# Optimization experiments

Measured on AMD Instinct MI355X. Metric: run time of the kernel, lower is better.

Reference implementation:

```python
import jax, jax.numpy as jnp
import numpy as np

N_NODES = 100000
N_EDGES = 1600000
N_GRAPHS = 512
IN_F, H1, H2 = 128, 128, 256
N_GROUPS, N_FAM = 16, 10


def setup_inputs() -> dict:
    key = jax.random.key(0)
    ks = jax.random.split(key, 8)
    x = jax.random.normal(ks[0], (N_NODES, IN_F), dtype=jnp.float32)
    edge_index = jax.random.randint(ks[1], (2, N_EDGES), 0, N_NODES, dtype=jnp.int64)
    batch = jnp.sort(jax.random.randint(ks[2], (N_NODES,), 0, N_GRAPHS, dtype=jnp.int64))
    W1 = jax.random.normal(ks[3], (IN_F, H1), dtype=jnp.float32) / np.sqrt(IN_F)
    b1 = jnp.zeros((H1,), dtype=jnp.float32)
    W2 = jax.random.normal(ks[4], (H1, H2), dtype=jnp.float32) / np.sqrt(H1)
    b2 = jnp.zeros((H2,), dtype=jnp.float32)
    Wg = jax.random.normal(ks[5], (H2, N_GROUPS), dtype=jnp.float32) / np.sqrt(H2)
    bg = jnp.zeros((N_GROUPS,), dtype=jnp.float32)
    Wf = jax.random.normal(ks[6], (N_GROUPS, H2, N_FAM), dtype=jnp.float32) / np.sqrt(H2)
    bf = jnp.zeros((N_GROUPS, N_FAM), dtype=jnp.float32)
    return {"x": x, "edge_index": edge_index, "batch": batch,
            "W1": W1, "b1": b1, "W2": W2, "b2": b2,
            "Wg": Wg, "bg": bg, "Wf": Wf, "bf": bf}


def gcn_conv(x, W, b, src, dst, num_nodes):
    # PyG GCNConv: add self-loops, symmetric normalization, scatter-add aggregation.
    xw = x @ W  # [N, out]
    deg = jax.ops.segment_sum(jnp.ones((src.shape[0],), x.dtype), dst,
                              num_segments=num_nodes) + 1.0  # +1 self-loop
    dinv = jax.lax.rsqrt(deg)
    coef = dinv[src] * dinv[dst]            # [E]
    msg = xw[src] * coef[:, None]           # gather + scale (memory-bound)
    agg = jax.ops.segment_sum(msg, dst, num_segments=num_nodes)
    agg = agg + xw * (dinv * dinv)[:, None]  # self-loop contribution
    return agg + b


def reference(x, edge_index, batch, W1, b1, W2, b2, Wg, bg, Wf, bf):
    src, dst = edge_index[0], edge_index[1]
    h = jax.nn.relu(gcn_conv(x, W1, b1, src, dst, N_NODES))
    # dropout p=0.5 is identity in eval mode
    h = gcn_conv(h, W2, b2, src, dst, N_NODES)
    # global mean pool over graphs
    sums = jax.ops.segment_sum(h, batch, num_segments=N_GRAPHS)       # [G, H2]
    cnts = jax.ops.segment_sum(jnp.ones((N_NODES,), h.dtype), batch,
                               num_segments=N_GRAPHS)
    pooled = sums / jnp.maximum(cnts, 1.0)[:, None]
    group_logits = pooled @ Wg + bg                                   # [G, num_groups]
    family_logits = jnp.einsum('bd,gdf->gbf', pooled, Wf) + bf[:, None, :]
    return group_logits, family_logits
```

## Files before the change

kernel.cpp:

```cpp
#include <hip/hip_runtime.h>

#define NN 100000
#define NE 1600000
#define NGR 512
#define KF 128
#define H2F 256
#define NGRP 16
#define NFAM 10

#define CH 128
#define NCHUNK ((NN + CH - 1) / CH)
#define PT 6656
#define NT ((NE + PT - 1) / PT)
#define PREPB_BLKS 64

#define NSPLIT 8

typedef __attribute__((ext_vector_type(8))) short short8;
typedef __attribute__((ext_vector_type(4))) float floatx4;
typedef __attribute__((ext_vector_type(2))) float floatx2;

__device__ __forceinline__ unsigned short f2bf(float f) {
  unsigned u = __float_as_uint(f);
  unsigned r = (u + 0x7fff + ((u >> 16) & 1)) >> 16;
  return (unsigned short)r;
}
__device__ __forceinline__ unsigned short pk_fp8(float a, float b) {
  return (unsigned short)__builtin_amdgcn_cvt_pk_fp8_f32(a, b, 0, false);
}
__device__ __forceinline__ floatx2 unpk_fp8(unsigned short u) {
  return __builtin_amdgcn_cvt_pk_f32_fp8((int)u, false);
}


__global__ __launch_bounds__(256) void k_histprep(const int* __restrict__ ei,
                                                  int* __restrict__ tot,
                                                  const float* __restrict__ W,
                                                  unsigned short* __restrict__ Bp) {
  __shared__ int lh[NCHUNK];
  int tid = threadIdx.x;
  if (blockIdx.x >= NT) {
    int idx = (blockIdx.x - NT) * 256 + tid;
    int j = idx & 7;
    int l = (idx >> 3) & 63;
    int rest = idx >> 9;
    int nc = rest & 7;
    int kc = rest >> 3;
    int k = kc * 32 + (l >> 4) * 8 + j;
    int nn = nc * 16 + (l & 15);
    Bp[idx] = f2bf(W[k * KF + nn]);
    return;
  }
  for (int g = tid; g < NCHUNK; g += 256) lh[g] = 0;
  __syncthreads();
  int base = blockIdx.x * PT;
  int nv = min(PT, NE - base);
  for (int i = tid; i < nv; i += 256) atomicAdd(&lh[ei[NE + base + i] >> 7], 1);
  __syncthreads();
  for (int g = tid; g < NCHUNK; g += 256) {
    int v = lh[g];
    if (v) atomicAdd(&tot[g], v);
  }
}


__global__ __launch_bounds__(256) void k_scantot(const int* __restrict__ tot,
                                                 int* __restrict__ cbase,
                                                 int* __restrict__ cursor) {
  __shared__ int ssc[256];
  int tid = threadIdx.x;
  int v4[4]; int loc = 0;
#pragma unroll
  for (int j = 0; j < 4; ++j) {
    int idx = tid * 4 + j;
    v4[j] = (idx < NCHUNK) ? tot[idx] : 0;
    loc += v4[j];
  }
  ssc[tid] = loc;
  __syncthreads();
  for (int off = 1; off < 256; off <<= 1) {
    int val = (tid >= off) ? ssc[tid - off] : 0;
    __syncthreads();
    ssc[tid] += val;
    __syncthreads();
  }
  int excl = ssc[tid] - loc;
#pragma unroll
  for (int j = 0; j < 4; ++j) {
    int idx = tid * 4 + j;
    if (idx < NCHUNK) { cbase[idx] = excl; cursor[idx] = excl; }
    excl += v4[j];
  }
  if (tid == 255) cbase[NCHUNK] = excl;
}


__global__ __launch_bounds__(256) void k_pscatter(const int* __restrict__ ei,
                                                  int* __restrict__ cursor,
                                                  int2* __restrict__ erec) {
  __shared__ int2 stage[PT];
  __shared__ int lstart[NCHUNK];
  __shared__ int lrun[NCHUNK];
  __shared__ int gbase[NCHUNK];
  __shared__ int ssc[256];
  int t0 = blockIdx.x, tid = threadIdx.x;
  for (int g = tid; g < NCHUNK; g += 256) lrun[g] = 0;
  __syncthreads();
  int base = t0 * PT;
  int nv = min(PT, NE - base);
  for (int i = tid; i < nv; i += 256) atomicAdd(&lrun[ei[NE + base + i] >> 7], 1);
  __syncthreads();
  int v4[4]; int loc = 0;
#pragma unroll
  for (int j = 0; j < 4; ++j) {
    int idx = tid * 4 + j;
    v4[j] = (idx < NCHUNK) ? lrun[idx] : 0;
    loc += v4[j];
  }
  ssc[tid] = loc;
  __syncthreads();
  for (int off = 1; off < 256; off <<= 1) {
    int val = (tid >= off) ? ssc[tid - off] : 0;
    __syncthreads();
    ssc[tid] += val;
    __syncthreads();
  }
  int excl = ssc[tid] - loc;
#pragma unroll
  for (int j = 0; j < 4; ++j) {
    int idx = tid * 4 + j;
    if (idx < NCHUNK) lstart[idx] = excl;
    excl += v4[j];
  }
  __syncthreads();
  for (int g = tid; g < NCHUNK; g += 256) {
    int cnt = ((g + 1 < NCHUNK) ? lstart[g + 1] : nv) - lstart[g];
    gbase[g] = cnt ? atomicAdd(&cursor[g], cnt) : 0;
    lrun[g] = lstart[g];
  }
  __syncthreads();
  for (int i = tid; i < nv; i += 256) {
    int s = ei[base + i], d = ei[NE + base + i];
    int pos = atomicAdd(&lrun[d >> 7], 1);
    stage[pos] = make_int2(s, d);
  }
  __syncthreads();
  for (int j = tid; j < nv; j += 256) {
    int2 r = stage[j];
    int g = r.y >> 7;
    erec[gbase[g] + (j - lstart[g])] = r;
  }
}


__global__ __launch_bounds__(256) void k_sort(const int2* __restrict__ erec,
                                              const int* __restrict__ cbase,
                                              int* __restrict__ esrc,
                                              float* __restrict__ ew,
                                              int* __restrict__ rowptr,
                                              float* __restrict__ dinv) {
  __shared__ int hist[CH];
  __shared__ int lrun[CH];
  __shared__ float ldv[CH];
  __shared__ int sc[256];
  const int c = blockIdx.x, tid = threadIdx.x;
  const int e0 = cbase[c], e1 = cbase[c + 1];
  const int nv = e1 - e0;
  if (tid < CH) hist[tid] = 0;
  __syncthreads();
  for (int i = tid; i < nv; i += 256) atomicAdd(&hist[erec[e0 + i].y & (CH - 1)], 1);
  __syncthreads();
  int deg = (tid < CH) ? hist[tid] : 0;
  sc[tid] = deg;
  __syncthreads();
  for (int off = 1; off < 256; off <<= 1) {
    int val = (tid >= off) ? sc[tid - off] : 0;
    __syncthreads();
    sc[tid] += val;
    __syncthreads();
  }
  int excl = sc[tid] - deg;
  int node = c * CH + tid;
  if (tid < CH) {
    lrun[tid] = excl;
    if (node < NN) {
      float dv = rsqrtf((float)(deg + 1));
      rowptr[node] = e0 + excl;
      dinv[node] = dv;
      ldv[tid] = dv;
    } else if (node == NN) {
      rowptr[NN] = e0 + excl;
    }
  }
  __syncthreads();
  for (int i = tid; i < nv; i += 256) {
    int2 r = erec[e0 + i];
    int ln = r.y & (CH - 1);
    int pos = atomicAdd(&lrun[ln], 1);
    esrc[e0 + pos] = r.x;
    ew[e0 + pos] = ldv[ln];
  }
}


__global__ __launch_bounds__(256) void k_gemm_mfma(const float* __restrict__ A,
                                                   const unsigned short* __restrict__ Bp,
                                                   const float* __restrict__ dinv,
                                                   unsigned short* __restrict__ C) {
  constexpr int K = 128;
  constexpr int NCH = KF / 16;
  const int wv = blockIdx.x * 4 + (threadIdx.x >> 6);
  const int row0 = wv * 16;
  if (row0 >= NN) return;
  const int lane = threadIdx.x & 63;
  const int m = lane & 15;
  const int q = lane >> 4;

  floatx4 acc[NCH];
#pragma unroll
  for (int i = 0; i < NCH; ++i) acc[i] = (floatx4){0.f, 0.f, 0.f, 0.f};

  const int arow = row0 + m;
#pragma unroll
  for (int kc = 0; kc < 4; ++kc) {
    const float* ap = A + (size_t)arow * K + kc * 32 + q * 8;
    float4 f0 = *(const float4*)ap;
    float4 f1 = *(const float4*)(ap + 4);
    short8 af;
    af[0] = (short)f2bf(f0.x); af[1] = (short)f2bf(f0.y);
    af[2] = (short)f2bf(f0.z); af[3] = (short)f2bf(f0.w);
    af[4] = (short)f2bf(f1.x); af[5] = (short)f2bf(f1.y);
    af[6] = (short)f2bf(f1.z); af[7] = (short)f2bf(f1.w);
    const unsigned short* bp = Bp + (size_t)kc * NCH * 512;
#pragma unroll
    for (int nc = 0; nc < NCH; ++nc) {
      short8 bfr = *(const short8*)(bp + (size_t)nc * 512 + lane * 8);
      acc[nc] = __builtin_amdgcn_mfma_f32_16x16x32_bf16(af, bfr, acc[nc], 0, 0, 0);
    }
  }

  float ds[4];
#pragma unroll
  for (int r = 0; r < 4; ++r) ds[r] = dinv[row0 + q * 4 + r];
#pragma unroll
  for (int nc = 0; nc < 4; ++nc) {
#pragma unroll
    for (int r = 0; r < 4; ++r) {
      int row = row0 + q * 4 + r;
      C[(size_t)row * 64 + nc * 16 + m] =
          pk_fp8(acc[nc][r] * ds[r], acc[nc + 4][r] * ds[r]);
    }
  }
}


__global__ __launch_bounds__(128) void k_agg1(const unsigned short* __restrict__ p,
                                              const float* __restrict__ bias,
                                              const int* __restrict__ rowptr,
                                              const int* __restrict__ esrc,
                                              const float* __restrict__ dinv,
                                              unsigned short* __restrict__ outp) {
  const int n = blockIdx.x * 2 + (threadIdx.x >> 6);
  const int t = threadIdx.x & 63;
  const int u = t & 31;
  const int half = t >> 5;
  const unsigned* __restrict__ prow = (const unsigned*)p;

  float a0 = 0.f, a1 = 0.f, a2 = 0.f, a3 = 0.f;

  if (half == 0) {
    unsigned v = prow[((unsigned)n << 5) + u];
    floatx2 lo = unpk_fp8((unsigned short)(v & 0xffffu));
    floatx2 hi = unpk_fp8((unsigned short)(v >> 16));
    a0 = lo.x; a1 = lo.y; a2 = hi.x; a3 = hi.y;
  }

  const int r0 = rowptr[n];
  const int r1 = rowptr[n + 1];
  int i = r0;

#define PAIR_TIER(NP)                                                  \
  for (; i + 2 * (NP) <= r1; i += 2 * (NP)) {                          \
    const int ib = i + half;                                           \
    unsigned s[NP];                                                    \
    _Pragma("unroll") for (int j = 0; j < (NP); ++j)                   \
        s[j] = (unsigned)esrc[ib + 2 * j];                             \
    unsigned v[NP];                                                    \
    _Pragma("unroll") for (int j = 0; j < (NP); ++j)                   \
        v[j] = prow[(s[j] << 5) + u];                                  \
    _Pragma("unroll") for (int j = 0; j < (NP); ++j) {                 \
      floatx2 lo = unpk_fp8((unsigned short)(v[j] & 0xffffu));         \
      floatx2 hi = unpk_fp8((unsigned short)(v[j] >> 16));             \
      a0 += lo.x; a1 += lo.y; a2 += hi.x; a3 += hi.y;                  \
    }                                                                  \
  }

  PAIR_TIER(8)
  PAIR_TIER(4)
  PAIR_TIER(2)
  PAIR_TIER(1)
#undef PAIR_TIER

  if (i < r1 && half == 0) {
    unsigned s = (unsigned)esrc[i];
    unsigned v = prow[(s << 5) + u];
    floatx2 lo = unpk_fp8((unsigned short)(v & 0xffffu));
    floatx2 hi = unpk_fp8((unsigned short)(v >> 16));
    a0 += lo.x; a1 += lo.y; a2 += hi.x; a3 += hi.y;
  }

  a0 += __shfl_down(a0, 32, 64);
  a1 += __shfl_down(a1, 32, 64);
  a2 += __shfl_down(a2, 32, 64);
  a3 += __shfl_down(a3, 32, 64);

  if (half == 0) {
    const float dn = dinv[n];
    float2 blo = *(const float2*)(bias + 2 * u);
    float2 bhi = *(const float2*)(bias + 64 + 2 * u);
    float x0 = fmaxf(fmaf(dn, a0, blo.x), 0.f) * dn;
    float x1 = fmaxf(fmaf(dn, a1, bhi.x), 0.f) * dn;
    float x2 = fmaxf(fmaf(dn, a2, blo.y), 0.f) * dn;
    float x3 = fmaxf(fmaf(dn, a3, bhi.y), 0.f) * dn;
    unsigned lo = pk_fp8(x0, x1);
    unsigned hi = pk_fp8(x2, x3);
    ((unsigned*)outp)[((unsigned)n << 5) + u] = lo | (hi << 16);
  }
}


__global__ __launch_bounds__(256) void k_aggpart(const unsigned short* __restrict__ p,
                                                 const int* __restrict__ batch,
                                                 const int* __restrict__ rowptr,
                                                 const int* __restrict__ esrc,
                                                 const float* __restrict__ ew,
                                                 const float* __restrict__ dinv,
                                                 float* __restrict__ pooled) {
  __shared__ float sacc[4][128];
  __shared__ int bnd[2];
  const int g = blockIdx.x / NSPLIT;
  const int part = blockIdx.x % NSPLIT;
  const int tid = threadIdx.x;
  if (tid < 2) {
    int target = g + tid;
    int lo = 0, hi = NN;
    while (lo < hi) { int mid = (lo + hi) >> 1; if (batch[mid] < target) lo = mid + 1; else hi = mid; }
    bnd[tid] = lo;
  }
  __syncthreads();
  const int start = bnd[0], end = bnd[1];
  const int wv = tid >> 6, t = tid & 63, u = t & 31, half = t >> 5;
  const unsigned* __restrict__ prow = (const unsigned*)p;

  float a0 = 0.f, a1 = 0.f, a2 = 0.f, a3 = 0.f;

  const int e0 = rowptr[start];
  const int e1 = rowptr[end];
  const int elen = e1 - e0;
  const int eper = (elen + NSPLIT - 1) / NSPLIT;
  const int is = min(e0 + part * eper, e1);
  const int ie = min(is + eper, e1);

  int i = is + wv * 2 + half;
  for (; i + 56 < ie; i += 64) {
    unsigned s[8];
    float w[8];
    unsigned v[8];
#pragma unroll
    for (int j = 0; j < 8; ++j) s[j] = (unsigned)esrc[i + 8 * j];
#pragma unroll
    for (int j = 0; j < 8; ++j) w[j] = ew[i + 8 * j];
#pragma unroll
    for (int j = 0; j < 8; ++j) v[j] = prow[(s[j] << 5) + u];
#pragma unroll
    for (int j = 0; j < 8; ++j) {
      floatx2 lo = unpk_fp8((unsigned short)(v[j] & 0xffffu));
      floatx2 hi = unpk_fp8((unsigned short)(v[j] >> 16));
      a0 = fmaf(w[j], lo.x, a0); a1 = fmaf(w[j], lo.y, a1);
      a2 = fmaf(w[j], hi.x, a2); a3 = fmaf(w[j], hi.y, a3);
    }
  }
  for (; i < ie; i += 8) {
    unsigned s_ = (unsigned)esrc[i];
    float w_ = ew[i];
    unsigned v_ = prow[(s_ << 5) + u];
    floatx2 lo = unpk_fp8((unsigned short)(v_ & 0xffffu));
    floatx2 hi = unpk_fp8((unsigned short)(v_ >> 16));
    a0 = fmaf(w_, lo.x, a0); a1 = fmaf(w_, lo.y, a1);
    a2 = fmaf(w_, hi.x, a2); a3 = fmaf(w_, hi.y, a3);
  }

  const int nlen = end - start;
  const int nper = (nlen + NSPLIT - 1) / NSPLIT;
  const int ns = min(start + part * nper, end);
  const int ne = min(ns + nper, end);
  for (int n = ns + wv * 2 + half; n < ne; n += 8) {
    float w_ = dinv[n];
    unsigned v_ = prow[((unsigned)n << 5) + u];
    floatx2 lo = unpk_fp8((unsigned short)(v_ & 0xffffu));
    floatx2 hi = unpk_fp8((unsigned short)(v_ >> 16));
    a0 = fmaf(w_, lo.x, a0); a1 = fmaf(w_, lo.y, a1);
    a2 = fmaf(w_, hi.x, a2); a3 = fmaf(w_, hi.y, a3);
  }

  a0 += __shfl_down(a0, 32, 64);
  a1 += __shfl_down(a1, 32, 64);
  a2 += __shfl_down(a2, 32, 64);
  a3 += __shfl_down(a3, 32, 64);
  if (half == 0) {
    sacc[wv][2 * u] = a0;
    sacc[wv][2 * u + 1] = a2;
    sacc[wv][2 * u + 64] = a1;
    sacc[wv][2 * u + 65] = a3;
  }
  __syncthreads();
  if (tid < KF) {
    float v = sacc[0][tid] + sacc[1][tid] + sacc[2][tid] + sacc[3][tid];
    atomicAdd(&pooled[(size_t)g * KF + tid], v);
  }
}


__global__ __launch_bounds__(256) void k_heads(const float* __restrict__ pooled,
                                               const int* __restrict__ batch,
                                               const float* __restrict__ W2,
                                               const float* __restrict__ b2,
                                               const float* __restrict__ Wg,
                                               const float* __restrict__ bg,
                                               const float* __restrict__ Wf,
                                               const float* __restrict__ bfb,
                                               float* __restrict__ out) {
  __shared__ float pr[KF];
  __shared__ float pp[H2F];
  __shared__ int bnd[2];
  const int g = blockIdx.x;
  const int tid = threadIdx.x;
  if (tid < 2) {
    int target = g + tid;
    int lo = 0, hi = NN;
    while (lo < hi) { int mid = (lo + hi) >> 1; if (batch[mid] < target) lo = mid + 1; else hi = mid; }
    bnd[tid] = lo;
  }
  __syncthreads();
  if (tid < KF) {
    float c = fmaxf((float)(bnd[1] - bnd[0]), 1.f);
    pr[tid] = pooled[(size_t)g * KF + tid] / c;
  }
  __syncthreads();
  float acc = b2[tid];
#pragma unroll 8
  for (int d = 0; d < KF; ++d) acc = fmaf(pr[d], W2[d * H2F + tid], acc);
  pp[tid] = acc;
  __syncthreads();
  if (tid < NGRP) {
    float a = bg[tid];
    for (int d = 0; d < H2F; ++d) a = fmaf(pp[d], Wg[d * NGRP + tid], a);
    out[g * NGRP + tid] = a;
  } else if (tid >= 64 && tid < 64 + NGRP * NFAM) {
    int uu = tid - 64;
    int gg = uu / NFAM;
    int ff = uu % NFAM;
    float a = bfb[gg * NFAM + ff];
    for (int d = 0; d < H2F; ++d) a = fmaf(pp[d], Wf[(gg * H2F + d) * NFAM + ff], a);
    out[NGR * NGRP + (size_t)gg * NGR * NFAM + g * NFAM + ff] = a;
  }
}


extern "C" void kernel_launch(void* const* d_in, const int* in_sizes, int n_in,
                              void* d_out, int out_size, void* d_ws, size_t ws_size,
                              hipStream_t stream) {
  const float* x    = (const float*)d_in[0];
  const int*   ei   = (const int*)d_in[1];
  const int*   batch= (const int*)d_in[2];
  const float* W1   = (const float*)d_in[3];
  const float* b1   = (const float*)d_in[4];
  const float* W2   = (const float*)d_in[5];
  const float* b2   = (const float*)d_in[6];
  const float* Wg   = (const float*)d_in[7];
  const float* bg   = (const float*)d_in[8];
  const float* Wf   = (const float*)d_in[9];
  const float* bfb  = (const float*)d_in[10];
  float* out = (float*)d_out;

  char* w = (char*)d_ws;
  auto take = [&](size_t bytes) {
    char* p = w;
    w += (bytes + 255) & ~(size_t)255;
    return (void*)p;
  };
  int*   tot   = (int*)take((size_t)NCHUNK * 4);
  float* pooled= (float*)take((size_t)NGR * KF * 4);
  int*   cbase = (int*)take((size_t)(NCHUNK + 1) * 4);
  int*   cursor= (int*)take((size_t)NCHUNK * 4);
  int2*  erec  = (int2*)take((size_t)NE * 8);
  int*   esrc  = (int*)take((size_t)NE * 4);
  float* ew    = (float*)take((size_t)NE * 4);
  int*   rowptr= (int*)take((size_t)(NN + 1) * 4);
  float* dinv  = (float*)take((size_t)NN * 4);
  unsigned short* Bp1 = (unsigned short*)take((size_t)KF * KF * 2);
  unsigned short* xw1 = (unsigned short*)take((size_t)NN * 64 * 2);
  unsigned short* h1  = (unsigned short*)take((size_t)NN * 64 * 2);

  size_t zbytes = (size_t)((char*)pooled - (char*)tot) + (size_t)NGR * KF * 4;
  hipMemsetAsync(tot, 0, zbytes, stream);

  k_histprep<<<NT + PREPB_BLKS, 256, 0, stream>>>(ei, tot, W1, Bp1);
  k_scantot<<<1, 256, 0, stream>>>(tot, cbase, cursor);
  k_pscatter<<<NT, 256, 0, stream>>>(ei, cursor, erec);
  k_sort<<<NCHUNK, 256, 0, stream>>>(erec, cbase, esrc, ew, rowptr, dinv);

  k_gemm_mfma<<<1563, 256, 0, stream>>>(x, Bp1, dinv, xw1);

  k_agg1<<<NN / 2, 128, 0, stream>>>(xw1, b1, rowptr, esrc, dinv, h1);
  k_aggpart<<<NGR * NSPLIT, 256, 0, stream>>>(h1, batch, rowptr, esrc, ew, dinv, pooled);
  k_heads<<<NGR, 256, 0, stream>>>(pooled, batch, W2, b2, Wg, bg, Wf, bfb, out);
}
```

Baseline: 292.4 us.

## Drop per-edge weight array, factor dinv per destination, precompute graph boundaries

Removes the per-edge weight array written by the sort kernel. The second aggregation now walks destination nodes via rowptr, sums the unscaled neighbour rows and multiplies once by dinv[dst], which saves one 4-byte read and write per edge. Graph boundary offsets are computed once by extra blocks in the histogram kernel instead of a binary search in every aggregation and heads block. The trade-off is that node-parallel work splitting within each graph replaces even edge-range splitting, which can leave load imbalance across high-degree nodes and uses half-wave pairing with tiered unrolling.

```diff
diff --git a/kernel.cpp b/kernel.cpp
--- a/kernel.cpp
+++ b/kernel.cpp
@@ -13,6 +13,7 @@
 #define PT 6656
 #define NT ((NE + PT - 1) / PT)
 #define PREPB_BLKS 64
+#define GBB ((NN + 255) / 256)
 
 #define NSPLIT 8
 
@@ -34,11 +35,24 @@
 
 
 __global__ __launch_bounds__(256) void k_histprep(const int* __restrict__ ei,
+                                                  const int* __restrict__ batch,
                                                   int* __restrict__ tot,
+                                                  int* __restrict__ gb,
                                                   const float* __restrict__ W,
                                                   unsigned short* __restrict__ Bp) {
   __shared__ int lh[NCHUNK];
   int tid = threadIdx.x;
+  if (blockIdx.x >= NT + PREPB_BLKS) {
+    int n = (blockIdx.x - NT - PREPB_BLKS) * 256 + tid;
+    if (n >= NN) return;
+    int b0 = batch[n];
+    if (n == 0) {
+      for (int g = 0; g <= b0; ++g) gb[g] = 0;
+    }
+    int b1 = (n + 1 < NN) ? batch[n + 1] : NGR;
+    for (int g = b0 + 1; g <= b1; ++g) gb[g] = n + 1;
+    return;
+  }
   if (blockIdx.x >= NT) {
     int idx = (blockIdx.x - NT) * 256 + tid;
     int j = idx & 7;
@@ -156,12 +170,10 @@
 __global__ __launch_bounds__(256) void k_sort(const int2* __restrict__ erec,
                                               const int* __restrict__ cbase,
                                               int* __restrict__ esrc,
-                                              float* __restrict__ ew,
                                               int* __restrict__ rowptr,
                                               float* __restrict__ dinv) {
   __shared__ int hist[CH];
   __shared__ int lrun[CH];
-  __shared__ float ldv[CH];
   __shared__ int sc[256];
   const int c = blockIdx.x, tid = threadIdx.x;
   const int e0 = cbase[c], e1 = cbase[c + 1];
@@ -184,10 +196,8 @@
   if (tid < CH) {
     lrun[tid] = excl;
     if (node < NN) {
-      float dv = rsqrtf((float)(deg + 1));
       rowptr[node] = e0 + excl;
-      dinv[node] = dv;
-      ldv[tid] = dv;
+      dinv[node] = rsqrtf((float)(deg + 1));
     } else if (node == NN) {
       rowptr[NN] = e0 + excl;
     }
@@ -195,10 +205,8 @@
   __syncthreads();
   for (int i = tid; i < nv; i += 256) {
     int2 r = erec[e0 + i];
-    int ln = r.y & (CH - 1);
-    int pos = atomicAdd(&lrun[ln], 1);
+    int pos = atomicAdd(&lrun[r.y & (CH - 1)], 1);
     esrc[e0 + pos] = r.x;
-    ew[e0 + pos] = ldv[ln];
   }
 }
 
@@ -330,77 +338,73 @@
 
 
 __global__ __launch_bounds__(256) void k_aggpart(const unsigned short* __restrict__ p,
-                                                 const int* __restrict__ batch,
+                                                 const int* __restrict__ gb,
                                                  const int* __restrict__ rowptr,
                                                  const int* __restrict__ esrc,
-                                                 const float* __restrict__ ew,
                                                  const float* __restrict__ dinv,
                                                  float* __restrict__ pooled) {
   __shared__ float sacc[4][128];
-  __shared__ int bnd[2];
   const int g = blockIdx.x / NSPLIT;
   const int part = blockIdx.x % NSPLIT;
   const int tid = threadIdx.x;
-  if (tid < 2) {
-    int target = g + tid;
-    int lo = 0, hi = NN;
-    while (lo < hi) { int mid = (lo + hi) >> 1; if (batch[mid] < target) lo = mid + 1; else hi = mid; }
-    bnd[tid] = lo;
-  }
-  __syncthreads();
-  const int start = bnd[0], end = bnd[1];
+  const int start = gb[g], end = gb[g + 1];
   const int wv = tid >> 6, t = tid & 63, u = t & 31, half = t >> 5;
   const unsigned* __restrict__ prow = (const unsigned*)p;
 
   float a0 = 0.f, a1 = 0.f, a2 = 0.f, a3 = 0.f;
-
-  const int e0 = rowptr[start];
-  const int e1 = rowptr[end];
-  const int elen = e1 - e0;
-  const int eper = (elen + NSPLIT - 1) / NSPLIT;
-  const int is = min(e0 + part * eper, e1);
-  const int ie = min(is + eper, e1);
-
-  int i = is + wv * 2 + half;
-  for (; i + 56 < ie; i += 64) {
-    unsigned s[8];
-    float w[8];
-    unsigned v[8];
-#pragma unroll
-    for (int j = 0; j < 8; ++j) s[j] = (unsigned)esrc[i + 8 * j];
-#pragma unroll
-    for (int j = 0; j < 8; ++j) w[j] = ew[i + 8 * j];
-#pragma unroll
-    for (int j = 0; j < 8; ++j) v[j] = prow[(s[j] << 5) + u];
-#pragma unroll
-    for (int j = 0; j < 8; ++j) {
-      floatx2 lo = unpk_fp8((unsigned short)(v[j] & 0xffffu));
-      floatx2 hi = unpk_fp8((unsigned short)(v[j] >> 16));
-      a0 = fmaf(w[j], lo.x, a0); a1 = fmaf(w[j], lo.y, a1);
-      a2 = fmaf(w[j], hi.x, a2); a3 = fmaf(w[j], hi.y, a3);
-    }
-  }
-  for (; i < ie; i += 8) {
-    unsigned s_ = (unsigned)esrc[i];
-    float w_ = ew[i];
-    unsigned v_ = prow[(s_ << 5) + u];
-    floatx2 lo = unpk_fp8((unsigned short)(v_ & 0xffffu));
-    floatx2 hi = unpk_fp8((unsigned short)(v_ >> 16));
-    a0 = fmaf(w_, lo.x, a0); a1 = fmaf(w_, lo.y, a1);
-    a2 = fmaf(w_, hi.x, a2); a3 = fmaf(w_, hi.y, a3);
-  }
 
   const int nlen = end - start;
   const int nper = (nlen + NSPLIT - 1) / NSPLIT;
   const int ns = min(start + part * nper, end);
   const int ne = min(ns + nper, end);
-  for (int n = ns + wv * 2 + half; n < ne; n += 8) {
-    float w_ = dinv[n];
-    unsigned v_ = prow[((unsigned)n << 5) + u];
-    floatx2 lo = unpk_fp8((unsigned short)(v_ & 0xffffu));
-    floatx2 hi = unpk_fp8((unsigned short)(v_ >> 16));
-    a0 = fmaf(w_, lo.x, a0); a1 = fmaf(w_, lo.y, a1);
-    a2 = fmaf(w_, hi.x, a2); a3 = fmaf(w_, hi.y, a3);
+
+  for (int n = ns + wv; n < ne; n += 4) {
+    float t0, t1, t2, t3;
+    if (half == 0) {
+      unsigned v = prow[((unsigned)n << 5) + u];
+      floatx2 lo = unpk_fp8((unsigned short)(v & 0xffffu));
+      floatx2 hi = unpk_fp8((unsigned short)(v >> 16));
+      t0 = lo.x; t1 = lo.y; t2 = hi.x; t3 = hi.y;
+    } else {
+      t0 = 0.f; t1 = 0.f; t2 = 0.f; t3 = 0.f;
+    }
+    const int r0 = rowptr[n];
+    const int r1 = rowptr[n + 1];
+    int i = r0;
+
+#define PAIR_TIER(NP)                                                  \
+    for (; i + 2 * (NP) <= r1; i += 2 * (NP)) {                        \
+      const int ib = i + half;                                         \
+      unsigned s[NP];                                                  \
+      _Pragma("unroll") for (int j = 0; j < (NP); ++j)                 \
+          s[j] = (unsigned)esrc[ib + 2 * j];                           \
+      unsigned v[NP];                                                  \
+      _Pragma("unroll") for (int j = 0; j < (NP); ++j)                 \
+          v[j] = prow[(s[j] << 5) + u];                                \
+      _Pragma("unroll") for (int j = 0; j < (NP); ++j) {               \
+        floatx2 lo = unpk_fp8((unsigned short)(v[j] & 0xffffu));       \
+        floatx2 hi = unpk_fp8((unsigned short)(v[j] >> 16));           \
+        t0 += lo.x; t1 += lo.y; t2 += hi.x; t3 += hi.y;                \
+      }                                                                \
+    }
+
+    PAIR_TIER(8)
+    PAIR_TIER(4)
+    PAIR_TIER(2)
+    PAIR_TIER(1)
+#undef PAIR_TIER
+
+    if (i < r1 && half == 0) {
+      unsigned s = (unsigned)esrc[i];
+      unsigned v = prow[(s << 5) + u];
+      floatx2 lo = unpk_fp8((unsigned short)(v & 0xffffu));
+      floatx2 hi = unpk_fp8((unsigned short)(v >> 16));
+      t0 += lo.x; t1 += lo.y; t2 += hi.x; t3 += hi.y;
+    }
+
+    const float dn = dinv[n];
+    a0 = fmaf(dn, t0, a0); a1 = fmaf(dn, t1, a1);
+    a2 = fmaf(dn, t2, a2); a3 = fmaf(dn, t3, a3);
   }
 
   a0 += __shfl_down(a0, 32, 64);
@@ -422,7 +426,7 @@
 
 
 __global__ __launch_bounds__(256) void k_heads(const float* __restrict__ pooled,
-                                               const int* __restrict__ batch,
+                                               const int* __restrict__ gb,
                                                const float* __restrict__ W2,
                                                const float* __restrict__ b2,
                                                const float* __restrict__ Wg,
@@ -432,18 +436,10 @@
                                                float* __restrict__ out) {
   __shared__ float pr[KF];
   __shared__ float pp[H2F];
-  __shared__ int bnd[2];
   const int g = blockIdx.x;
   const int tid = threadIdx.x;
-  if (tid < 2) {
-    int target = g + tid;
-    int lo = 0, hi = NN;
-    while (lo < hi) { int mid = (lo + hi) >> 1; if (batch[mid] < target) lo = mid + 1; else hi = mid; }
-    bnd[tid] = lo;
-  }
-  __syncthreads();
   if (tid < KF) {
-    float c = fmaxf((float)(bnd[1] - bnd[0]), 1.f);
+    float c = fmaxf((float)(gb[g + 1] - gb[g]), 1.f);
     pr[tid] = pooled[(size_t)g * KF + tid] / c;
   }
   __syncthreads();
@@ -491,11 +487,11 @@
   };
   int*   tot   = (int*)take((size_t)NCHUNK * 4);
   float* pooled= (float*)take((size_t)NGR * KF * 4);
+  int*   gb    = (int*)take((size_t)(NGR + 1) * 4);
   int*   cbase = (int*)take((size_t)(NCHUNK + 1) * 4);
   int*   cursor= (int*)take((size_t)NCHUNK * 4);
   int2*  erec  = (int2*)take((size_t)NE * 8);
   int*   esrc  = (int*)take((size_t)NE * 4);
-  float* ew    = (float*)take((size_t)NE * 4);
   int*   rowptr= (int*)take((size_t)(NN + 1) * 4);
   float* dinv  = (float*)take((size_t)NN * 4);
   unsigned short* Bp1 = (unsigned short*)take((size_t)KF * KF * 2);
@@ -505,14 +501,14 @@
   size_t zbytes = (size_t)((char*)pooled - (char*)tot) + (size_t)NGR * KF * 4;
   hipMemsetAsync(tot, 0, zbytes, stream);
 
-  k_histprep<<<NT + PREPB_BLKS, 256, 0, stream>>>(ei, tot, W1, Bp1);
+  k_histprep<<<NT + PREPB_BLKS + GBB, 256, 0, stream>>>(ei, batch, tot, gb, W1, Bp1);
   k_scantot<<<1, 256, 0, stream>>>(tot, cbase, cursor);
   k_pscatter<<<NT, 256, 0, stream>>>(ei, cursor, erec);
-  k_sort<<<NCHUNK, 256, 0, stream>>>(erec, cbase, esrc, ew, rowptr, dinv);
+  k_sort<<<NCHUNK, 256, 0, stream>>>(erec, cbase, esrc, rowptr, dinv);
 
   k_gemm_mfma<<<1563, 256, 0, stream>>>(x, Bp1, dinv, xw1);
 
   k_agg1<<<NN / 2, 128, 0, stream>>>(xw1, b1, rowptr, esrc, dinv, h1);
-  k_aggpart<<<NGR * NSPLIT, 256, 0, stream>>>(h1, batch, rowptr, esrc, ew, dinv, pooled);
-  k_heads<<<NGR, 256, 0, stream>>>(pooled, batch, W2, b2, Wg, bg, Wf, bfb, out);
-}
+  k_aggpart<<<NGR * NSPLIT, 256, 0, stream>>>(h1, gb, rowptr, esrc, dinv, pooled);
+  k_heads<<<NGR, 256, 0, stream>>>(pooled, gb, W2, b2, Wg, bg, Wf, bfb, out);
+}
```

New measurement: 292.6 us. No clear change (+0.1%).
